# Optimization experiments

Measured on AMD Instinct MI355X. Metric: run time of the kernel, lower is better.

Reference implementation:

```python
import jax, jax.numpy as jnp
import numpy as np

LR = 1e-4   # learning_rate from init
EPS = 1e-8


def setup_inputs() -> dict:
    key = jax.random.key(0)
    k1, k2 = jax.random.split(key)
    N, K, F = 8192, 8192, 4096
    return {
        "x": jax.random.normal(k1, (N, F), jnp.float32),
        "centroids": jax.random.normal(k2, (K, F), jnp.float32),
        "m": jnp.zeros((K,), jnp.float32),
        "v": jnp.zeros((K,), jnp.float32),
        "betas": jnp.array([0.9, 0.999, 1.0, 1.0], jnp.float32),
        "step": 1,
    }


def reference(x, centroids, m, v, betas, step):
    N = x.shape[0]
    K = centroids.shape[0]
    dt = x.dtype
    # dist[k, n] = ||x_n - c_k||^2, via norm expansion (same math as sum((x-c)^2))
    xn = jnp.sum(x * x, axis=1)                    # [N]
    cn = jnp.sum(centroids * centroids, axis=1)    # [K]
    dist = cn[:, None] + xn[None, :] - 2.0 * (centroids @ x.T)  # [K, N]
    nearest = jnp.argmin(dist, axis=0)             # [N]
    # point_loss = sum(dist[:, nearest]) / N ; sum over K of gathered cols == gather of colsums
    colsum = jnp.sum(dist, axis=0)                 # [N]
    point_loss = jnp.sum(colsum[nearest]) / N
    # sum_{i,j} ||c_i - c_j||^2 = 2K*sum||c||^2 - 2*||sum_i c_i||^2 (includes zero diagonal)
    csum = jnp.sum(centroids, axis=0)
    centroid_loss = 1.0 / (2.0 * K * jnp.sum(cn) - 2.0 * jnp.sum(csum * csum))
    # per-cluster segment reduce replaces the Python loop over K
    counts = jax.ops.segment_sum(jnp.ones((N,), dt), nearest, num_segments=K)  # [K]
    sums = jax.ops.segment_sum(x, nearest, num_segments=K)                     # [K, F]
    nonempty = counts > 0
    new_center = sums / jnp.maximum(counts, 1.0)[:, None]
    delta = jnp.where(nonempty, jnp.sum((new_center - centroids) ** 2, axis=1), 0.0)  # [K]
    delta_k = jnp.sum(nonempty.astype(dt))
    sum_delta = jnp.sum(delta)
    # Adam-style per-cluster state update (only for non-empty clusters)
    g = delta + betas[2] * point_loss + betas[3] * centroid_loss
    m_new = jnp.where(nonempty, betas[0] * m + (1.0 - betas[0]) * g, m)
    v_new = jnp.where(nonempty, betas[1] * v + (1.0 - betas[1]) * g * g, v)
    mh = m_new / (1.0 - betas[0] ** step)
    vh = v_new / (1.0 - betas[1] ** step)
    upd = LR * mh / (jnp.sqrt(vh) + EPS)
    next_centroids = jnp.where(nonempty[:, None], centroids - upd[:, None], centroids)
    return sum_delta / delta_k, point_loss, centroid_loss, next_centroids, m_new, v_new
```

## Files before the change

kernel.cpp:

```cpp
#include <hip/hip_runtime.h>
#include <stdint.h>

#define KCL 8192
#define NPT 8192
#define FD  4096
#define KF  33554432
#define LRC 1e-4f
#define EPSC 1e-8f
#define SLAB 1024
#define BK  32

typedef float  f32x4 __attribute__((ext_vector_type(4)));
typedef __fp16 h8    __attribute__((ext_vector_type(8)));
typedef __fp16 h4    __attribute__((ext_vector_type(4)));

struct Scal {
  float Scn;
  float csum2;
  float cl;
  float pl_sum;
  float sum_delta;
  int   nonempty;
};

__device__ __forceinline__ void gload16(const void* g, void* l) {
  __builtin_amdgcn_global_load_lds((const __attribute__((address_space(1))) void*)g,
                                   (__attribute__((address_space(3))) void*)l, 16, 0, 0);
}

__device__ __forceinline__ float wave_sum(float v) {
  #pragma unroll
  for (int m = 1; m < 64; m <<= 1) v += __shfl_xor(v, m, 64);
  return v;
}
__device__ __forceinline__ double wave_sum(double v) {
  #pragma unroll
  for (int m = 1; m < 64; m <<= 1) v += __shfl_xor(v, m, 64);
  return v;
}

__global__ __launch_bounds__(256) void rownorm_k(const float* __restrict__ src,
                                                 double* __restrict__ norms) {
  __shared__ double sred[4];
  const int r = blockIdx.x, t = threadIdx.x;
  const f32x4* row = (const f32x4*)(src + (size_t)r * FD);
  double ss = 0.0;
  #pragma unroll
  for (int q = 0; q < 4; ++q) {
    f32x4 v = row[q * 256 + t];
    ss += (double)(v[0]*v[0] + v[1]*v[1]) + (double)(v[2]*v[2] + v[3]*v[3]);
  }
  ss = wave_sum(ss);
  int wave = t >> 6, lane = t & 63;
  if (lane == 0) sred[wave] = ss;
  __syncthreads();
  if (t == 0) norms[r] = sred[0] + sred[1] + sred[2] + sred[3];
}

template<bool WITH_DOT>
__global__ __launch_bounds__(256) void prep_rows(
    const float* __restrict__ src, __fp16* __restrict__ hi, __fp16* __restrict__ lo,
    const float* __restrict__ csum, float* __restrict__ colsum, const Scal* __restrict__ sc)
{
  __shared__ double sred[4], sred2[4];
  const int r = blockIdx.x, t = threadIdx.x;
  const size_t rb = (size_t)r * FD;
  const f32x4* row = (const f32x4*)(src + rb);
  double ss = 0.0, dd = 0.0;
  #pragma unroll
  for (int q = 0; q < 4; ++q) {
    int c4 = q * 256 + t;
    f32x4 v = row[c4];
    h4 hv = __builtin_convertvector(v, h4);
    f32x4 hb = __builtin_convertvector(hv, f32x4);
    h4 lv = __builtin_convertvector(v - hb, h4);
    *(h4*)(hi + rb + (size_t)c4 * 4) = hv;
    *(h4*)(lo + rb + (size_t)c4 * 4) = lv;
    if (WITH_DOT) {
      ss += (double)(v[0]*v[0] + v[1]*v[1]) + (double)(v[2]*v[2] + v[3]*v[3]);
      f32x4 cs = *(const f32x4*)(csum + c4 * 4);
      dd += (double)(v[0]*cs[0] + v[1]*cs[1]) + (double)(v[2]*cs[2] + v[3]*cs[3]);
    }
  }
  if (WITH_DOT) {
    ss = wave_sum(ss); dd = wave_sum(dd);
    int wave = t >> 6, lane = t & 63;
    if (lane == 0) { sred[wave] = ss; sred2[wave] = dd; }
    __syncthreads();
    if (t == 0) {
      double S = sred[0] + sred[1] + sred[2] + sred[3];
      double D = sred2[0] + sred2[1] + sred2[2] + sred2[3];
      colsum[r] = (float)((double)sc->Scn + (double)KCL * S - 2.0 * D);
    }
  }
}

__global__ __launch_bounds__(256) void csum_part_k(const float* __restrict__ c,
                                                   float* __restrict__ parts) {
  int f = blockIdx.x * 256 + threadIdx.x;
  int r0 = blockIdx.y * 256;
  float s = 0.f;
  for (int i = 0; i < 256; ++i) s += c[(size_t)(r0 + i) * FD + f];
  parts[(size_t)blockIdx.y * FD + f] = s;
}

__global__ __launch_bounds__(256) void csum_reduce_k(const float* __restrict__ parts,
                                                     float* __restrict__ csum, Scal* sc,
                                                     int nparts) {
  int f = blockIdx.x * 256 + threadIdx.x;
  float s = 0.f;
  for (int j = 0; j < nparts; ++j) s += parts[(size_t)j * FD + f];
  csum[f] = s;
  float sq = wave_sum(s * s);
  __shared__ float sr[4];
  int wave = threadIdx.x >> 6, lane = threadIdx.x & 63;
  if (lane == 0) sr[wave] = sq;
  __syncthreads();
  if (threadIdx.x == 0) atomicAdd(&sc->csum2, sr[0] + sr[1] + sr[2] + sr[3]);
}

__global__ __launch_bounds__(256) void cn_reduce_k(const double* __restrict__ cn, Scal* sc) {
  double s = 0.0;
  for (int i = threadIdx.x; i < KCL; i += 256) s += cn[i];
  s = wave_sum(s);
  __shared__ double sr[4];
  int wave = threadIdx.x >> 6, lane = threadIdx.x & 63;
  if (lane == 0) sr[wave] = s;
  __syncthreads();
  if (threadIdx.x == 0) {
    double S = sr[0] + sr[1] + sr[2] + sr[3];
    sc->Scn = (float)S;
    sc->cl = (float)(1.0 / (2.0 * (double)KCL * S - 2.0 * (double)sc->csum2));
  }
}

__global__ __launch_bounds__(512, 2) void gemm_argmin_k(
    const __fp16* __restrict__ Ahi, const __fp16* __restrict__ Alo,
    const __fp16* __restrict__ Bhi, const __fp16* __restrict__ Blo,
    const double* __restrict__ cn,
    double* __restrict__ part_val, int* __restrict__ part_idx,
    int kglob0, int nglob0, int swz)
{
  __shared__ __fp16 tile[2 * 4 * 8192];

  const int tid  = threadIdx.x;
  const int lane = tid & 63;
  const int w    = tid >> 6;
  const int wr   = w >> 2, wc = w & 3;
  const int ln15 = lane & 15, lc = lane >> 4;

  int kb, nb;
  if (swz) {
    int xcd = blockIdx.x & 7, idx = blockIdx.x >> 3;
    int st = idx >> 5, i = idx & 31;
    kb = (st & 1) * 16 + (i & 15);
    nb = (st >> 1) * 16 + xcd * 2 + (i >> 4);
  } else {
    kb = blockIdx.y; nb = blockIdx.x;
  }
  const int k0l = kb * 256, n0l = nb * 256;
  const int k0g = kglob0 + k0l, n0g = nglob0 + n0l;

  const __fp16* gAh = Ahi + (size_t)k0l * FD;
  const __fp16* gAl = Alo + (size_t)k0l * FD;
  const __fp16* gBh = Bhi + (size_t)n0l * FD;
  const __fp16* gBl = Blo + (size_t)n0l * FD;

  const int c0 = tid,        r0 = c0 >> 2, sc0 = (c0 & 3) ^ ((r0 >> 1) & 3);
  const int c1 = tid + 512,  r1 = c1 >> 2, sc1 = (c1 & 3) ^ ((r1 >> 1) & 3);
  const size_t gof0 = (size_t)r0 * FD + sc0 * 8;
  const size_t gof1 = (size_t)r1 * FD + sc1 * 8;

  #define TBUF(buf, arr) (tile + (((buf) * 4 + (arr)) << 13))
  #define STAGE(gsrc, buf, arr, fo) do { \
    gload16((gsrc) + gof0 + (fo), TBUF(buf, arr) + c0 * 8); \
    gload16((gsrc) + gof1 + (fo), TBUF(buf, arr) + c1 * 8); } while (0)

  const int pcs = (lc ^ ((ln15 >> 1) & 3)) * 8;
  const int abase = wr * 128 + ln15;
  const int bbase = wc * 64 + ln15;

  f32x4 acc[8][4] = {};
  h8 ah[8], bh[4];

  STAGE(gAh, 0, 0, 0); STAGE(gBh, 0, 2, 0); STAGE(gAl, 0, 1, 0); STAGE(gBl, 0, 3, 0);
  asm volatile("s_waitcnt vmcnt(0)" ::: "memory");
  __builtin_amdgcn_s_barrier();

  for (int t = 0; t < FD / BK; ++t) {
    const int cur = t & 1, nxt = cur ^ 1;
    const size_t fo = (size_t)(t + 1) * BK;
    const bool st = (t < FD / BK - 1);

    {
      const __fp16* sA = TBUF(cur, 0);
      const __fp16* sB = TBUF(cur, 2);
      #pragma unroll
      for (int m = 0; m < 8; ++m) ah[m] = *(const h8*)(sA + (abase + m * 16) * 32 + pcs);
      #pragma unroll
      for (int n = 0; n < 4; ++n) bh[n] = *(const h8*)(sB + (bbase + n * 16) * 32 + pcs);
    }
    if (st) STAGE(gAh, nxt, 0, fo);
    __builtin_amdgcn_s_setprio(1);
    #pragma unroll
    for (int m = 0; m < 8; ++m)
      #pragma unroll
      for (int n = 0; n < 4; ++n)
        acc[m][n] = __builtin_amdgcn_mfma_f32_16x16x32_f16(ah[m], bh[n], acc[m][n], 0, 0, 0);
    __builtin_amdgcn_s_setprio(0);
    if (st) asm volatile("s_waitcnt vmcnt(2)" ::: "memory");
    else    asm volatile("s_waitcnt vmcnt(0)" ::: "memory");
    __builtin_amdgcn_sched_barrier(0);
    __builtin_amdgcn_s_barrier();

    {
      h8 bl[4];
      const __fp16* sB = TBUF(cur, 3);
      #pragma unroll
      for (int n = 0; n < 4; ++n) bl[n] = *(const h8*)(sB + (bbase + n * 16) * 32 + pcs);
      if (st) STAGE(gBh, nxt, 2, fo);
      __builtin_amdgcn_s_setprio(1);
      #pragma unroll
      for (int m = 0; m < 8; ++m)
        #pragma unroll
        for (int n = 0; n < 4; ++n)
          acc[m][n] = __builtin_amdgcn_mfma_f32_16x16x32_f16(ah[m], bl[n], acc[m][n], 0, 0, 0);
      __builtin_amdgcn_s_setprio(0);
    }

    {
      h8 al[8];
      const __fp16* sA = TBUF(cur, 1);
      #pragma unroll
      for (int m = 0; m < 8; ++m) al[m] = *(const h8*)(sA + (abase + m * 16) * 32 + pcs);
      if (st) { STAGE(gAl, nxt, 1, fo); STAGE(gBl, nxt, 3, fo); }
      __builtin_amdgcn_s_setprio(1);
      #pragma unroll
      for (int m = 0; m < 8; ++m)
        #pragma unroll
        for (int n = 0; n < 4; ++n)
          acc[m][n] = __builtin_amdgcn_mfma_f32_16x16x32_f16(al[m], bh[n], acc[m][n], 0, 0, 0);
      __builtin_amdgcn_s_setprio(0);
      asm volatile("s_waitcnt vmcnt(4)" ::: "memory");
      __builtin_amdgcn_sched_barrier(0);
      __builtin_amdgcn_s_barrier();
    }
  }

  double* eCn = (double*)tile;
  double* eV  = (double*)(tile + 1024);
  int*    eI  = (int*)(tile + 3072);
  __syncthreads();
  if (tid < 256) eCn[tid] = cn[k0g + tid];
  __syncthreads();

  #pragma unroll
  for (int n = 0; n < 4; ++n) {
    double bv = 1e300; int bi = 0x7fffffff;
    #pragma unroll
    for (int m = 0; m < 8; ++m)
      #pragma unroll
      for (int j = 0; j < 4; ++j) {
        int kl = wr * 128 + m * 16 + lc * 4 + j;
        double d = eCn[kl] - 2.0 * (double)acc[m][n][j];
        if (d < bv || (d == bv && kl < bi)) { bv = d; bi = kl; }
      }
    #pragma unroll
    for (int mask = 16; mask < 64; mask <<= 1) {
      double ov = __shfl_xor(bv, mask, 64);
      int    oi = __shfl_xor(bi, mask, 64);
      if (ov < bv || (ov == bv && oi < bi)) { bv = ov; bi = oi; }
    }
    if (lc == 0) {
      int col = wc * 64 + n * 16 + ln15;
      eV[wr * 256 + col] = bv; eI[wr * 256 + col] = bi;
    }
  }
  __syncthreads();
  if (tid < 256) {
    double v0 = eV[tid]; int i0 = eI[tid];
    double v1 = eV[256 + tid]; int i1 = eI[256 + tid];
    if (v1 < v0 || (v1 == v0 && i1 < i0)) { v0 = v1; i0 = i1; }
    part_val[(size_t)(k0g >> 8) * NPT + n0g + tid] = v0;
    part_idx[(size_t)(k0g >> 8) * NPT + n0g + tid] = i0 + k0g;
  }
  #undef TBUF
  #undef STAGE
}

__global__ __launch_bounds__(256) void nearest_k(
    const double* __restrict__ part_val, const int* __restrict__ part_idx,
    const float* __restrict__ colsum, int* __restrict__ nearest,
    int* __restrict__ counts, Scal* sc)
{
  int n = blockIdx.x * 256 + threadIdx.x;
  double bv = 1e300; int bi = 0x7fffffff;
  for (int kb = 0; kb < 32; ++kb) {
    double v = part_val[(size_t)kb * NPT + n];
    int    i = part_idx[(size_t)kb * NPT + n];
    if (v < bv || (v == bv && i < bi)) { bv = v; bi = i; }
  }
  nearest[n] = bi;
  atomicAdd(&counts[bi], 1);
  float pls = wave_sum(colsum[bi]);
  __shared__ float sr[4];
  int wave = threadIdx.x >> 6, lane = threadIdx.x & 63;
  if (lane == 0) sr[wave] = pls;
  __syncthreads();
  if (threadIdx.x == 0) atomicAdd(&sc->pl_sum, sr[0] + sr[1] + sr[2] + sr[3]);
}

__global__ __launch_bounds__(256) void scan_k(const int* __restrict__ counts,
                                              int* __restrict__ offsets) {
  __shared__ int s[256];
  int t = threadIdx.x;
  int base = t * 32;
  int sum = 0;
  for (int i = 0; i < 32; ++i) sum += counts[base + i];
  s[t] = sum; __syncthreads();
  for (int off = 1; off < 256; off <<= 1) {
    int v = (t >= off) ? s[t - off] : 0;
    __syncthreads();
    s[t] += v;
    __syncthreads();
  }
  int run = s[t] - sum;
  for (int i = 0; i < 32; ++i) { offsets[base + i] = run; run += counts[base + i]; }
}

__global__ __launch_bounds__(256) void fill_k(const int* __restrict__ nearest,
                                              const int* __restrict__ offsets,
                                              int* __restrict__ cursor, int* __restrict__ list) {
  int n = blockIdx.x * 256 + threadIdx.x;
  int k = nearest[n];
  int p = atomicAdd(&cursor[k], 1);
  list[offsets[k] + p] = n;
}

__global__ __launch_bounds__(256) void cluster_adam_k(
    const float* __restrict__ x, const float* __restrict__ cen,
    const float* __restrict__ m_in, const float* __restrict__ v_in,
    const float* __restrict__ betas, const int* __restrict__ step,
    const int* __restrict__ counts, const int* __restrict__ offsets,
    const int* __restrict__ list, Scal* sc, float* __restrict__ out)
{
  const int k = blockIdx.x, t = threadIdx.x;
  const int cnt = counts[k];
  const size_t kb = (size_t)k * FD;
  const f32x4* crow = (const f32x4*)(cen + kb);
  f32x4 c4[4];
  #pragma unroll
  for (int q = 0; q < 4; ++q) c4[q] = crow[q * 256 + t];

  float mn, vn, u;
  if (cnt > 0) {
    f32x4 acc[4] = {};
    const int off = offsets[k];
    for (int i = 0; i < cnt; ++i) {
      const f32x4* row = (const f32x4*)(x + (size_t)list[off + i] * FD);
      #pragma unroll
      for (int q = 0; q < 4; ++q) acc[q] += row[q * 256 + t];
    }
    float part = 0.f;
    const float fc = (float)cnt;
    #pragma unroll
    for (int q = 0; q < 4; ++q)
      #pragma unroll
      for (int j = 0; j < 4; ++j) {
        float d = acc[q][j] / fc - c4[q][j];
        part += d * d;
      }
    part = wave_sum(part);
    __shared__ float sr[4];
    __shared__ float sdelta;
    int wave = t >> 6, lane = t & 63;
    if (lane == 0) sr[wave] = part;
    __syncthreads();
    if (t == 0) {
      float dsum = sr[0] + sr[1] + sr[2] + sr[3];
      sdelta = dsum;
      atomicAdd(&sc->sum_delta, dsum);
      atomicAdd(&sc->nonempty, 1);
    }
    __syncthreads();
    float delta_k = sdelta;
    float b0 = betas[0], b1 = betas[1], b2 = betas[2], b3 = betas[3];
    float pl = sc->pl_sum / (float)NPT;
    float g = delta_k + b2 * pl + b3 * sc->cl;
    mn = b0 * m_in[k] + (1.f - b0) * g;
    vn = b1 * v_in[k] + (1.f - b1) * g * g;
    int st = *step;
    float mh = mn / (1.f - powf(b0, (float)st));
    float vh = vn / (1.f - powf(b1, (float)st));
    u = LRC * mh / (sqrtf(vh) + EPSC);
  } else {
    mn = m_in[k]; vn = v_in[k]; u = 0.f;
  }
  if (t == 0) {
    out[3 + (size_t)KF + k] = mn;
    out[3 + (size_t)KF + KCL + k] = vn;
  }
  float* orow = out + 3 + kb;
  #pragma unroll
  for (int q = 0; q < 4; ++q) {
    f32x4 o = c4[q] - u;
    *(f32x4*)(orow + (size_t)(q * 256 + t) * 4) = o;
  }
}

__global__ void finalize_k(const Scal* __restrict__ sc, float* __restrict__ out) {
  out[0] = sc->sum_delta / (float)sc->nonempty;
  out[1] = sc->pl_sum / (float)NPT;
  out[2] = sc->cl;
}

extern "C" void kernel_launch(void* const* d_in, const int* in_sizes, int n_in,
                              void* d_out, int out_size, void* d_ws, size_t ws_size,
                              hipStream_t stream) {
  const float* x     = (const float*)d_in[0];
  const float* cen   = (const float*)d_in[1];
  const float* m_in  = (const float*)d_in[2];
  const float* v_in  = (const float*)d_in[3];
  const float* betas = (const float*)d_in[4];
  const int*   step  = (const int*)d_in[5];
  float* out = (float*)d_out;

  char* p = (char*)d_ws;
  auto alloc = [&](size_t b) { char* r = p; p += (b + 255) & ~(size_t)255; return r; };
  Scal* sc      = (Scal*)alloc(sizeof(Scal));
  int* counts   = (int*)alloc(KCL * 4);
  int* cursor   = (int*)alloc(KCL * 4);
  size_t zlen   = (size_t)(p - (char*)d_ws);
  int* offsets  = (int*)alloc(KCL * 4);
  int* list     = (int*)alloc(NPT * 4);
  int* nearest  = (int*)alloc(NPT * 4);
  double* cn    = (double*)alloc(KCL * 8);
  float* colsum = (float*)alloc(NPT * 4);
  float* csum   = (float*)alloc(FD * 4);
  float* cparts = (float*)alloc((size_t)32 * FD * 4);
  double* pval  = (double*)alloc((size_t)32 * NPT * 8);
  int*   pidx   = (int*)alloc((size_t)32 * NPT * 4);
  const bool fast = ws_size >= (size_t)280 * 1024 * 1024;
  const size_t splitRows = fast ? (size_t)KCL : (size_t)SLAB;
  __fp16* chi = (__fp16*)alloc(splitRows * FD * 2);
  __fp16* clo = (__fp16*)alloc(splitRows * FD * 2);
  __fp16* xhi = (__fp16*)alloc(splitRows * FD * 2);
  __fp16* xlo = (__fp16*)alloc(splitRows * FD * 2);
  (void)in_sizes; (void)n_in; (void)out_size;

  hipMemsetAsync(d_ws, 0, zlen, stream);

  rownorm_k<<<KCL, 256, 0, stream>>>(cen, cn);
  csum_part_k<<<dim3(16, 32), 256, 0, stream>>>(cen, cparts);
  csum_reduce_k<<<16, 256, 0, stream>>>(cparts, csum, sc, 32);
  cn_reduce_k<<<1, 256, 0, stream>>>(cn, sc);

  if (fast) {
    prep_rows<false><<<KCL, 256, 0, stream>>>(cen, chi, clo, nullptr, nullptr, nullptr);
    prep_rows<true><<<NPT, 256, 0, stream>>>(x, xhi, xlo, csum, colsum, sc);
    gemm_argmin_k<<<1024, 512, 0, stream>>>(chi, clo, xhi, xlo, cn, pval, pidx, 0, 0, 1);
  } else {
    for (int q = 0; q < NPT / SLAB; ++q) {
      prep_rows<true><<<SLAB, 256, 0, stream>>>(x + (size_t)q * SLAB * FD, xhi, xlo,
                                                csum, colsum + q * SLAB, sc);
      for (int pp = 0; pp < KCL / SLAB; ++pp) {
        prep_rows<false><<<SLAB, 256, 0, stream>>>(cen + (size_t)pp * SLAB * FD, chi, clo,
                                                   nullptr, nullptr, nullptr);
        gemm_argmin_k<<<dim3(SLAB / 256, SLAB / 256), 512, 0, stream>>>(
            chi, clo, xhi, xlo, cn, pval, pidx, pp * SLAB, q * SLAB, 0);
      }
    }
  }

  nearest_k<<<NPT / 256, 256, 0, stream>>>(pval, pidx, colsum, nearest, counts, sc);
  scan_k<<<1, 256, 0, stream>>>(counts, offsets);
  fill_k<<<NPT / 256, 256, 0, stream>>>(nearest, offsets, cursor, list);
  cluster_adam_k<<<KCL, 256, 0, stream>>>(x, cen, m_in, v_in, betas, step,
                                          counts, offsets, list, sc, out);
  finalize_k<<<1, 1, 0, stream>>>(sc, out);
}
```

Baseline: 1.663 ms.

## Fuse centroid row norms into prep pass and consolidate GEMM staging barriers

The centroid row-norm computation moves into the fp16 hi/lo split kernel on the fast path, which drops the separate rownorm_k launch and its extra full read of the centroid matrix. In the GEMM main loop, all four next-tile global-to-LDS stages are now issued at the start of the iteration, and the two intermediate waitcnt/barrier pairs become a single full wait and barrier at the end. This cuts synchronisation points per K-step but issues more loads at once and removes the staggered overlap, which may raise register or latency pressure.

```diff
diff --git a/kernel.cpp b/kernel.cpp
--- a/kernel.cpp
+++ b/kernel.cpp
@@ -57,10 +57,11 @@
   if (t == 0) norms[r] = sred[0] + sred[1] + sred[2] + sred[3];
 }
 
-template<bool WITH_DOT>
+template<bool WITH_DOT, bool WNORM>
 __global__ __launch_bounds__(256) void prep_rows(
     const float* __restrict__ src, __fp16* __restrict__ hi, __fp16* __restrict__ lo,
-    const float* __restrict__ csum, float* __restrict__ colsum, const Scal* __restrict__ sc)
+    double* __restrict__ norms, const float* __restrict__ csum,
+    float* __restrict__ colsum, const Scal* __restrict__ sc)
 {
   __shared__ double sred[4], sred2[4];
   const int r = blockIdx.x, t = threadIdx.x;
@@ -76,21 +77,26 @@
     h4 lv = __builtin_convertvector(v - hb, h4);
     *(h4*)(hi + rb + (size_t)c4 * 4) = hv;
     *(h4*)(lo + rb + (size_t)c4 * 4) = lv;
+    if (WITH_DOT || WNORM)
+      ss += (double)(v[0]*v[0] + v[1]*v[1]) + (double)(v[2]*v[2] + v[3]*v[3]);
     if (WITH_DOT) {
-      ss += (double)(v[0]*v[0] + v[1]*v[1]) + (double)(v[2]*v[2] + v[3]*v[3]);
       f32x4 cs = *(const f32x4*)(csum + c4 * 4);
       dd += (double)(v[0]*cs[0] + v[1]*cs[1]) + (double)(v[2]*cs[2] + v[3]*cs[3]);
     }
   }
-  if (WITH_DOT) {
-    ss = wave_sum(ss); dd = wave_sum(dd);
+  if (WITH_DOT || WNORM) {
+    ss = wave_sum(ss);
+    if (WITH_DOT) dd = wave_sum(dd);
     int wave = t >> 6, lane = t & 63;
-    if (lane == 0) { sred[wave] = ss; sred2[wave] = dd; }
+    if (lane == 0) { sred[wave] = ss; if (WITH_DOT) sred2[wave] = dd; }
     __syncthreads();
     if (t == 0) {
       double S = sred[0] + sred[1] + sred[2] + sred[3];
-      double D = sred2[0] + sred2[1] + sred2[2] + sred2[3];
-      colsum[r] = (float)((double)sc->Scn + (double)KCL * S - 2.0 * D);
+      if (WNORM) norms[r] = S;
+      if (WITH_DOT) {
+        double D = sred2[0] + sred2[1] + sred2[2] + sred2[3];
+        colsum[r] = (float)((double)sc->Scn + (double)KCL * S - 2.0 * D);
+      }
     }
   }
 }
@@ -200,7 +206,8 @@
       #pragma unroll
       for (int n = 0; n < 4; ++n) bh[n] = *(const h8*)(sB + (bbase + n * 16) * 32 + pcs);
     }
-    if (st) STAGE(gAh, nxt, 0, fo);
+    if (st) { STAGE(gAh, nxt, 0, fo); STAGE(gBh, nxt, 2, fo);
+              STAGE(gAl, nxt, 1, fo); STAGE(gBl, nxt, 3, fo); }
     __builtin_amdgcn_s_setprio(1);
     #pragma unroll
     for (int m = 0; m < 8; ++m)
@@ -208,17 +215,12 @@
       for (int n = 0; n < 4; ++n)
         acc[m][n] = __builtin_amdgcn_mfma_f32_16x16x32_f16(ah[m], bh[n], acc[m][n], 0, 0, 0);
     __builtin_amdgcn_s_setprio(0);
-    if (st) asm volatile("s_waitcnt vmcnt(2)" ::: "memory");
-    else    asm volatile("s_waitcnt vmcnt(0)" ::: "memory");
-    __builtin_amdgcn_sched_barrier(0);
-    __builtin_amdgcn_s_barrier();
 
     {
       h8 bl[4];
       const __fp16* sB = TBUF(cur, 3);
       #pragma unroll
       for (int n = 0; n < 4; ++n) bl[n] = *(const h8*)(sB + (bbase + n * 16) * 32 + pcs);
-      if (st) STAGE(gBh, nxt, 2, fo);
       __builtin_amdgcn_s_setprio(1);
       #pragma unroll
       for (int m = 0; m < 8; ++m)
@@ -233,7 +235,6 @@
       const __fp16* sA = TBUF(cur, 1);
       #pragma unroll
       for (int m = 0; m < 8; ++m) al[m] = *(const h8*)(sA + (abase + m * 16) * 32 + pcs);
-      if (st) { STAGE(gAl, nxt, 1, fo); STAGE(gBl, nxt, 3, fo); }
       __builtin_amdgcn_s_setprio(1);
       #pragma unroll
       for (int m = 0; m < 8; ++m)
@@ -241,10 +242,11 @@
         for (int n = 0; n < 4; ++n)
           acc[m][n] = __builtin_amdgcn_mfma_f32_16x16x32_f16(al[m], bh[n], acc[m][n], 0, 0, 0);
       __builtin_amdgcn_s_setprio(0);
-      asm volatile("s_waitcnt vmcnt(4)" ::: "memory");
-      __builtin_amdgcn_sched_barrier(0);
-      __builtin_amdgcn_s_barrier();
-    }
+    }
+
+    asm volatile("s_waitcnt vmcnt(0)" ::: "memory");
+    __builtin_amdgcn_sched_barrier(0);
+    __builtin_amdgcn_s_barrier();
   }
 
   double* eCn = (double*)tile;
@@ -450,22 +452,24 @@
 
   hipMemsetAsync(d_ws, 0, zlen, stream);
 
-  rownorm_k<<<KCL, 256, 0, stream>>>(cen, cn);
-  csum_part_k<<<dim3(16, 32), 256, 0, stream>>>(cen, cparts);
-  csum_reduce_k<<<16, 256, 0, stream>>>(cparts, csum, sc, 32);
-  cn_reduce_k<<<1, 256, 0, stream>>>(cn, sc);
-
   if (fast) {
-    prep_rows<false><<<KCL, 256, 0, stream>>>(cen, chi, clo, nullptr, nullptr, nullptr);
-    prep_rows<true><<<NPT, 256, 0, stream>>>(x, xhi, xlo, csum, colsum, sc);
+    prep_rows<false, true><<<KCL, 256, 0, stream>>>(cen, chi, clo, cn, nullptr, nullptr, nullptr);
+    csum_part_k<<<dim3(16, 32), 256, 0, stream>>>(cen, cparts);
+    csum_reduce_k<<<16, 256, 0, stream>>>(cparts, csum, sc, 32);
+    cn_reduce_k<<<1, 256, 0, stream>>>(cn, sc);
+    prep_rows<true, false><<<NPT, 256, 0, stream>>>(x, xhi, xlo, nullptr, csum, colsum, sc);
     gemm_argmin_k<<<1024, 512, 0, stream>>>(chi, clo, xhi, xlo, cn, pval, pidx, 0, 0, 1);
   } else {
+    rownorm_k<<<KCL, 256, 0, stream>>>(cen, cn);
+    csum_part_k<<<dim3(16, 32), 256, 0, stream>>>(cen, cparts);
+    csum_reduce_k<<<16, 256, 0, stream>>>(cparts, csum, sc, 32);
+    cn_reduce_k<<<1, 256, 0, stream>>>(cn, sc);
     for (int q = 0; q < NPT / SLAB; ++q) {
-      prep_rows<true><<<SLAB, 256, 0, stream>>>(x + (size_t)q * SLAB * FD, xhi, xlo,
-                                                csum, colsum + q * SLAB, sc);
+      prep_rows<true, false><<<SLAB, 256, 0, stream>>>(x + (size_t)q * SLAB * FD, xhi, xlo,
+                                                       nullptr, csum, colsum + q * SLAB, sc);
       for (int pp = 0; pp < KCL / SLAB; ++pp) {
-        prep_rows<false><<<SLAB, 256, 0, stream>>>(cen + (size_t)pp * SLAB * FD, chi, clo,
-                                                   nullptr, nullptr, nullptr);
+        prep_rows<false, false><<<SLAB, 256, 0, stream>>>(cen + (size_t)pp * SLAB * FD, chi, clo,
+                                                          nullptr, nullptr, nullptr, nullptr);
         gemm_argmin_k<<<dim3(SLAB / 256, SLAB / 256), 512, 0, stream>>>(
             chi, clo, xhi, xlo, cn, pval, pidx, pp * SLAB, q * SLAB, 0);
       }
```

Result: slower. 1.715 ms (+3.1%).
